# Kernel tuning notes

Measured on AMD Instinct MI355X. Metric: run time of the kernel, lower is better.

The kernel has to match this reference:

```python
import jax, jax.numpy as jnp
import numpy as np

B, L, D, P = 2, 1024, 256, 32

def setup_inputs() -> dict:
    key = jax.random.key(0)
    k1, k2, k3, k4, k5 = jax.random.split(key, 5)
    x = jax.random.normal(k1, (B, L, D), dtype=jnp.float32)
    s_in = 1.0 / np.sqrt(D)
    W_phase = jax.random.normal(k2, (D, P), dtype=jnp.float32) * s_in
    b_phase = jax.random.normal(k3, (P,), dtype=jnp.float32) * 0.01
    W_val = jax.random.normal(k4, (D, D), dtype=jnp.float32) * s_in
    b_val = jax.random.normal(k5, (D,), dtype=jnp.float32) * 0.01
    return {"x": x, "W_phase": W_phase, "b_phase": b_phase, "W_val": W_val, "b_val": b_val}

def reference(x, W_phase, b_phase, W_val, b_val):
    # phases: [B, L, P] in (-pi, pi)
    phases = jnp.tanh(x @ W_phase + b_phase) * jnp.float32(np.pi)
    # unit-magnitude complex phasors: [B, L, P]
    phasors = jnp.exp(1j * phases)  # complex64
    # values: [B, L, D]
    values = x @ W_val + b_val
    # bind value vector to each phasor via outer product: [B, L, P, D] complex64
    bound = phasors[..., None] * values[:, :, None, :].astype(jnp.complex64)
    # holographic memory = running sum over sequence position
    memory = jnp.cumsum(bound, axis=1)
    return (memory, phases, phasors)
```

## Files before the change

### kernel.cpp

```cpp
#include <hip/hip_runtime.h>
#include <math.h>

#define B_ 2
#define L_ 1024
#define D_ 256
#define P_ 32
#define NROW (B_*L_)
#define C_ 16
#define CL_ (L_/C_)
#define PIF 3.14159265358979323846f

typedef float nvf4 __attribute__((ext_vector_type(4)));
typedef float nvf2 __attribute__((ext_vector_type(2)));

__global__ __launch_bounds__(256) void k_proj3(
    const float* __restrict__ x, const float* __restrict__ Wp,
    const float* __restrict__ bp, const float* __restrict__ Wv,
    const float* __restrict__ bv, float* __restrict__ values,
    float* __restrict__ phases_out, float* __restrict__ phasor_out,
    float2* __restrict__ phasorT, int phasorMode, int hasPT)
{
    __shared__ float smem[5120];
    const int tid = threadIdx.x;

    if (blockIdx.x < NROW / 4) {
        const int row0 = blockIdx.x * 4;
        float*  xsv = smem;
        float4* red = (float4*)(smem + 1024);

        ((float4*)xsv)[tid] = ((const float4*)(x + (size_t)row0 * D_))[tid];
        __syncthreads();

        const int q  = tid >> 6;
        const int c4 = tid & 63;
        const float4* Wv4 = (const float4*)Wv;
        float4 acc[4];
        #pragma unroll
        for (int r = 0; r < 4; ++r) acc[r] = make_float4(0.f, 0.f, 0.f, 0.f);

        const int k0 = q * 64;
        #pragma unroll 4
        for (int kk = 0; kk < 64; ++kk) {
            const int k = k0 + kk;
            float4 w = Wv4[k * 64 + c4];
            #pragma unroll
            for (int r = 0; r < 4; ++r) {
                float xv = xsv[r * D_ + k];
                acc[r].x += xv * w.x; acc[r].y += xv * w.y;
                acc[r].z += xv * w.z; acc[r].w += xv * w.w;
            }
        }
        #pragma unroll
        for (int r = 0; r < 4; ++r) red[(r * 4 + q) * 64 + c4] = acc[r];
        __syncthreads();

        const int r2 = tid >> 6;
        float4 s0 = red[(r2 * 4 + 0) * 64 + c4];
        float4 s1 = red[(r2 * 4 + 1) * 64 + c4];
        float4 s2 = red[(r2 * 4 + 2) * 64 + c4];
        float4 s3 = red[(r2 * 4 + 3) * 64 + c4];
        const float4 b4 = ((const float4*)bv)[c4];
        float4 out;
        out.x = s0.x + s1.x + s2.x + s3.x + b4.x;
        out.y = s0.y + s1.y + s2.y + s3.y + b4.y;
        out.z = s0.z + s1.z + s2.z + s3.z + b4.z;
        out.w = s0.w + s1.w + s2.w + s3.w + b4.w;
        ((float4*)values)[(size_t)(row0 + r2) * 64 + c4] = out;
    } else {
        const int row0 = (blockIdx.x - NROW / 4) * 8;
        float* xs = smem;
        const float4* xg4 = (const float4*)(x + (size_t)row0 * D_);
        ((float4*)xs)[tid]       = xg4[tid];
        ((float4*)xs)[tid + 256] = xg4[tid + 256];
        __syncthreads();

        const int p  = tid & (P_ - 1);
        const int rr = tid >> 5;
        const float* xr = xs + rr * D_;
        float a = 0.f;
        #pragma unroll 8
        for (int k = 0; k < D_; ++k)
            a += xr[k] * Wp[k * P_ + p];
        float ph = tanhf(a + bp[p]) * PIF;
        const int row = row0 + rr;
        const int idx = row * P_ + p;
        phases_out[idx] = ph;
        float s, c;
        sincosf(ph, &s, &c);
        if (phasorMode == 0) {
            ((float2*)phasor_out)[idx] = make_float2(c, s);
        } else if (phasorMode == 1) {
            phasor_out[idx] = c;
        }
        if (hasPT) {
            const int b = row >> 10, l = row & (L_ - 1);
            phasorT[(b * P_ + p) * L_ + l] = make_float2(c, s);
        }
    }
}

__global__ __launch_bounds__(128) void k_partial(
    const float* __restrict__ values, const float* __restrict__ phases,
    const float2* __restrict__ phasorT, float4* __restrict__ S4, int hasPT)
{
    const int blk = blockIdx.x;
    const int c = blk & (C_ - 1);
    const int p = (blk >> 4) & (P_ - 1);
    const int b = blk >> 9;
    const int tid = threadIdx.x;
    const int l0 = c * CL_;

    __shared__ float2 pc[CL_];
    if (tid < CL_) {
        if (hasPT) {
            pc[tid] = phasorT[(b * P_ + p) * L_ + l0 + tid];
        } else {
            float ph = phases[(b * L_ + l0 + tid) * P_ + p];
            pc[tid] = make_float2(__cosf(ph), __sinf(ph));
        }
    }
    __syncthreads();

    const float2* v2 = (const float2*)(values + (size_t)(b * L_ + l0) * D_);
    float4 acc = make_float4(0.f, 0.f, 0.f, 0.f);
    #pragma unroll 8
    for (int i = 0; i < CL_; ++i) {
        float2 ph = pc[i];
        float2 v  = v2[i * (D_/2) + tid];
        acc.x += ph.x * v.x;
        acc.y += ph.y * v.x;
        acc.z += ph.x * v.y;
        acc.w += ph.y * v.y;
    }
    S4[((b * P_ + p) * C_ + c) * (D_/2) + tid] = acc;
}

__global__ __launch_bounds__(128) void k_scan(
    const float* __restrict__ values, const float* __restrict__ phases,
    const float2* __restrict__ phasorT, const float4* __restrict__ S4,
    float* __restrict__ mem, int mode, int hasPT)
{
    const int blk = blockIdx.x;
    const int c = blk & (C_ - 1);
    const int p = (blk >> 4) & (P_ - 1);
    const int b = blk >> 9;
    const int tid = threadIdx.x;
    const int l0 = c * CL_;

    __shared__ float2 pc[CL_];
    if (tid < CL_) {
        if (hasPT) {
            pc[tid] = phasorT[(b * P_ + p) * L_ + l0 + tid];
        } else {
            float ph = phases[(b * L_ + l0 + tid) * P_ + p];
            pc[tid] = make_float2(__cosf(ph), __sinf(ph));
        }
    }

    float4 carry = make_float4(0.f, 0.f, 0.f, 0.f);
    const float4* Sbase = S4 + (size_t)(b * P_ + p) * C_ * (D_/2) + tid;
    for (int cc = 0; cc < c; ++cc) {
        float4 s = Sbase[cc * (D_/2)];
        carry.x += s.x; carry.y += s.y; carry.z += s.z; carry.w += s.w;
    }
    __syncthreads();

    const float2* v2 = (const float2*)(values + (size_t)(b * L_ + l0) * D_);
    #pragma unroll 8
    for (int i = 0; i < CL_; ++i) {
        float2 ph = pc[i];
        float2 v  = v2[i * (D_/2) + tid];
        carry.x += ph.x * v.x;
        carry.y += ph.y * v.x;
        carry.z += ph.x * v.y;
        carry.w += ph.y * v.y;
        const size_t rowIdx = (size_t)(b * L_ + l0 + i) * P_ + p;
        if (mode == 0) {
            nvf4 cv = { carry.x, carry.y, carry.z, carry.w };
            __builtin_nontemporal_store(cv, (nvf4*)mem + rowIdx * (D_/2) + tid);
        } else {
            nvf2 cv = { carry.x, carry.z };
            __builtin_nontemporal_store(cv, (nvf2*)mem + rowIdx * (D_/2) + tid);
        }
    }
}

__global__ __launch_bounds__(128) void k_scan_rc(
    const float* __restrict__ values, const float* __restrict__ phases,
    float* __restrict__ mem, int mode)
{
    const int blk = blockIdx.x;
    const int c = blk & (C_ - 1);
    const int p = (blk >> 4) & (P_ - 1);
    const int b = blk >> 9;
    const int tid = threadIdx.x;
    const int l0 = c * CL_;

    const float2* vb = (const float2*)(values + (size_t)b * L_ * D_);
    float4 carry = make_float4(0.f, 0.f, 0.f, 0.f);
    for (int l = 0; l < l0; ++l) {
        float ph = phases[(b * L_ + l) * P_ + p];
        float s = __sinf(ph), cs = __cosf(ph);
        float2 v = vb[l * (D_/2) + tid];
        carry.x += cs * v.x; carry.y += s * v.x;
        carry.z += cs * v.y; carry.w += s * v.y;
    }
    for (int i = 0; i < CL_; ++i) {
        const int l = l0 + i;
        float ph = phases[(b * L_ + l) * P_ + p];
        float s = __sinf(ph), cs = __cosf(ph);
        float2 v = vb[l * (D_/2) + tid];
        carry.x += cs * v.x; carry.y += s * v.x;
        carry.z += cs * v.y; carry.w += s * v.y;
        const size_t rowIdx = (size_t)(b * L_ + l) * P_ + p;
        if (mode == 0) ((float4*)mem)[rowIdx * (D_/2) + tid] = carry;
        else ((float2*)mem)[rowIdx * (D_/2) + tid] = make_float2(carry.x, carry.z);
    }
}

extern "C" void kernel_launch(void* const* d_in, const int* in_sizes, int n_in,
                              void* d_out, int out_size, void* d_ws, size_t ws_size,
                              hipStream_t stream) {
    const float* x  = (const float*)d_in[0];
    const float* Wp = (const float*)d_in[1];
    const float* bp = (const float*)d_in[2];
    const float* Wv = (const float*)d_in[3];
    const float* bv = (const float*)d_in[4];
    float* out = (float*)d_out;

    const size_t nMemF = (size_t)2 * B_ * L_ * P_ * D_;
    const size_t nMemR = (size_t)B_ * L_ * P_ * D_;
    const size_t nPh   = (size_t)B_ * L_ * P_;

    int mode; size_t memFloats;
    if ((size_t)out_size >= nMemF + 3 * nPh) { mode = 0; memFloats = nMemF; }
    else                                     { mode = 1; memFloats = nMemR; }
    const bool memFits      = (size_t)out_size >= memFloats;
    const bool phasesInOut  = (size_t)out_size >= memFloats + nPh;
    const bool phasorsInOut =
        (size_t)out_size >= memFloats + nPh + (mode == 0 ? 2 * nPh : nPh);

    const size_t valB = (size_t)B_ * L_ * D_ * sizeof(float);
    const size_t phB  = nPh * sizeof(float);
    const size_t s4B  = (size_t)B_ * P_ * C_ * (D_/2) * sizeof(float4);
    const size_t ptB  = (size_t)B_ * P_ * L_ * sizeof(float2);
    float*  values   = (float*)d_ws;
    float*  phasesWs = (float*)((char*)d_ws + valB);
    float4* S4       = (float4*)((char*)d_ws + valB + phB);
    float2* phasorT  = (float2*)((char*)d_ws + valB + phB + s4B);

    float* phasesPtr = phasesInOut ? (out + memFloats)
                     : (ws_size >= valB + phB ? phasesWs : nullptr);
    if (phasesPtr == nullptr) return;

    float* phasorPtr = phasorsInOut ? (out + memFloats + nPh) : nullptr;
    const int phasorMode = phasorsInOut ? mode : 2;

    const bool pathA = ws_size >= valB + phB + s4B;
    const int  hasPT = (pathA && ws_size >= valB + phB + s4B + ptB) ? 1 : 0;

    k_proj3<<<NROW / 4 + NROW / 8, 256, 0, stream>>>(
        x, Wp, bp, Wv, bv, values, phasesPtr, phasorPtr, phasorT,
        phasorMode, hasPT);
    if (!memFits) return;

    if (pathA) {
        k_partial<<<B_ * P_ * C_, 128, 0, stream>>>(values, phasesPtr, phasorT,
                                                    S4, hasPT);
        k_scan<<<B_ * P_ * C_, 128, 0, stream>>>(values, phasesPtr, phasorT,
                                                 S4, out, mode, hasPT);
    } else {
        k_scan_rc<<<B_ * P_ * C_, 128, 0, stream>>>(values, phasesPtr, out, mode);
    }
}
```

Before: 110.6 us.

## Fuse partial-sum and scan kernels by recomputing chunk prefix per block

Replaces the two-pass chunked scan (partial sums into a workspace buffer, then a scan kernel that reads them) with one kernel. Each block recomputes its prefix carry directly from values over all earlier positions, using phasors staged in shared memory. This removes one launch and the S4 round trip through global memory. In exchange, later chunks redo up to the full sequence length of multiply-adds and value reads, so the work per block is uneven. It also adds a real-only (cosine) phasor path for mode 1.

Measured after the change: 151.3 us. 36.8% more time.

```diff
diff --git a/kernel.cpp b/kernel.cpp
--- a/kernel.cpp
+++ b/kernel.cpp
@@ -18,7 +18,7 @@
     const float* __restrict__ bp, const float* __restrict__ Wv,
     const float* __restrict__ bv, float* __restrict__ values,
     float* __restrict__ phases_out, float* __restrict__ phasor_out,
-    float2* __restrict__ phasorT, int phasorMode, int hasPT)
+    float* __restrict__ phasorT, int phasorMode, int mode, int hasPT)
 {
     __shared__ float smem[5120];
     const int tid = threadIdx.x;
@@ -94,14 +94,17 @@
         }
         if (hasPT) {
             const int b = row >> 10, l = row & (L_ - 1);
-            phasorT[(b * P_ + p) * L_ + l] = make_float2(c, s);
+            const size_t ti = (size_t)(b * P_ + p) * L_ + l;
+            if (mode == 1) phasorT[ti] = c;
+            else ((float2*)phasorT)[ti] = make_float2(c, s);
         }
     }
 }
 
-__global__ __launch_bounds__(128) void k_partial(
+__global__ __launch_bounds__(128) void k_scan_fused(
     const float* __restrict__ values, const float* __restrict__ phases,
-    const float2* __restrict__ phasorT, float4* __restrict__ S4, int hasPT)
+    const float* __restrict__ phasorT, float* __restrict__ mem,
+    int mode, int hasPT)
 {
     const int blk = blockIdx.x;
     const int c = blk & (C_ - 1);
@@ -109,112 +112,78 @@
     const int b = blk >> 9;
     const int tid = threadIdx.x;
     const int l0 = c * CL_;
-
-    __shared__ float2 pc[CL_];
-    if (tid < CL_) {
-        if (hasPT) {
-            pc[tid] = phasorT[(b * P_ + p) * L_ + l0 + tid];
+    const int bp = b * P_ + p;
+    const int nPre = l0 + CL_;
+
+    __shared__ float2 pc2[L_];
+    float* pc1 = (float*)pc2;
+
+    if (hasPT) {
+        if (mode == 1) {
+            const float4* src = (const float4*)(phasorT + (size_t)bp * L_);
+            for (int i = tid; i < nPre / 4; i += 128)
+                ((float4*)pc1)[i] = src[i];
         } else {
-            float ph = phases[(b * L_ + l0 + tid) * P_ + p];
-            pc[tid] = make_float2(__cosf(ph), __sinf(ph));
+            const float4* src =
+                (const float4*)((const float2*)phasorT + (size_t)bp * L_);
+            for (int i = tid; i < nPre / 2; i += 128)
+                ((float4*)pc2)[i] = src[i];
+        }
+    } else {
+        for (int l = tid; l < nPre; l += 128) {
+            float ph = phases[(b * L_ + l) * P_ + p];
+            if (mode == 1) pc1[l] = __cosf(ph);
+            else           pc2[l] = make_float2(__cosf(ph), __sinf(ph));
         }
     }
     __syncthreads();
 
-    const float2* v2 = (const float2*)(values + (size_t)(b * L_ + l0) * D_);
-    float4 acc = make_float4(0.f, 0.f, 0.f, 0.f);
-    #pragma unroll 8
-    for (int i = 0; i < CL_; ++i) {
-        float2 ph = pc[i];
-        float2 v  = v2[i * (D_/2) + tid];
-        acc.x += ph.x * v.x;
-        acc.y += ph.y * v.x;
-        acc.z += ph.x * v.y;
-        acc.w += ph.y * v.y;
-    }
-    S4[((b * P_ + p) * C_ + c) * (D_/2) + tid] = acc;
-}
-
-__global__ __launch_bounds__(128) void k_scan(
-    const float* __restrict__ values, const float* __restrict__ phases,
-    const float2* __restrict__ phasorT, const float4* __restrict__ S4,
-    float* __restrict__ mem, int mode, int hasPT)
-{
-    const int blk = blockIdx.x;
-    const int c = blk & (C_ - 1);
-    const int p = (blk >> 4) & (P_ - 1);
-    const int b = blk >> 9;
-    const int tid = threadIdx.x;
-    const int l0 = c * CL_;
-
-    __shared__ float2 pc[CL_];
-    if (tid < CL_) {
-        if (hasPT) {
-            pc[tid] = phasorT[(b * P_ + p) * L_ + l0 + tid];
-        } else {
-            float ph = phases[(b * L_ + l0 + tid) * P_ + p];
-            pc[tid] = make_float2(__cosf(ph), __sinf(ph));
-        }
-    }
-
-    float4 carry = make_float4(0.f, 0.f, 0.f, 0.f);
-    const float4* Sbase = S4 + (size_t)(b * P_ + p) * C_ * (D_/2) + tid;
-    for (int cc = 0; cc < c; ++cc) {
-        float4 s = Sbase[cc * (D_/2)];
-        carry.x += s.x; carry.y += s.y; carry.z += s.z; carry.w += s.w;
-    }
-    __syncthreads();
-
-    const float2* v2 = (const float2*)(values + (size_t)(b * L_ + l0) * D_);
-    #pragma unroll 8
-    for (int i = 0; i < CL_; ++i) {
-        float2 ph = pc[i];
-        float2 v  = v2[i * (D_/2) + tid];
-        carry.x += ph.x * v.x;
-        carry.y += ph.y * v.x;
-        carry.z += ph.x * v.y;
-        carry.w += ph.y * v.y;
-        const size_t rowIdx = (size_t)(b * L_ + l0 + i) * P_ + p;
-        if (mode == 0) {
+    const float2* v2 = (const float2*)(values + (size_t)b * L_ * D_);
+
+    if (mode == 1) {
+        float cx = 0.f, cz = 0.f;
+        #pragma unroll 8
+        for (int l = 0; l < l0; ++l) {
+            float pcv = pc1[l];
+            float2 v  = v2[(size_t)l * (D_/2) + tid];
+            cx += pcv * v.x;
+            cz += pcv * v.y;
+        }
+        #pragma unroll 8
+        for (int i = 0; i < CL_; ++i) {
+            const int l = l0 + i;
+            float pcv = pc1[l];
+            float2 v  = v2[(size_t)l * (D_/2) + tid];
+            cx += pcv * v.x;
+            cz += pcv * v.y;
+            nvf2 cv = { cx, cz };
+            __builtin_nontemporal_store(
+                cv, (nvf2*)mem + ((size_t)(b * L_ + l) * P_ + p) * (D_/2) + tid);
+        }
+    } else {
+        float4 carry = make_float4(0.f, 0.f, 0.f, 0.f);
+        #pragma unroll 8
+        for (int l = 0; l < l0; ++l) {
+            float2 ph = pc2[l];
+            float2 v  = v2[(size_t)l * (D_/2) + tid];
+            carry.x += ph.x * v.x;
+            carry.y += ph.y * v.x;
+            carry.z += ph.x * v.y;
+            carry.w += ph.y * v.y;
+        }
+        #pragma unroll 8
+        for (int i = 0; i < CL_; ++i) {
+            const int l = l0 + i;
+            float2 ph = pc2[l];
+            float2 v  = v2[(size_t)l * (D_/2) + tid];
+            carry.x += ph.x * v.x;
+            carry.y += ph.y * v.x;
+            carry.z += ph.x * v.y;
+            carry.w += ph.y * v.y;
             nvf4 cv = { carry.x, carry.y, carry.z, carry.w };
-            __builtin_nontemporal_store(cv, (nvf4*)mem + rowIdx * (D_/2) + tid);
-        } else {
-            nvf2 cv = { carry.x, carry.z };
-            __builtin_nontemporal_store(cv, (nvf2*)mem + rowIdx * (D_/2) + tid);
-        }
-    }
-}
-
-__global__ __launch_bounds__(128) void k_scan_rc(
-    const float* __restrict__ values, const float* __restrict__ phases,
-    float* __restrict__ mem, int mode)
-{
-    const int blk = blockIdx.x;
-    const int c = blk & (C_ - 1);
-    const int p = (blk >> 4) & (P_ - 1);
-    const int b = blk >> 9;
-    const int tid = threadIdx.x;
-    const int l0 = c * CL_;
-
-    const float2* vb = (const float2*)(values + (size_t)b * L_ * D_);
-    float4 carry = make_float4(0.f, 0.f, 0.f, 0.f);
-    for (int l = 0; l < l0; ++l) {
-        float ph = phases[(b * L_ + l) * P_ + p];
-        float s = __sinf(ph), cs = __cosf(ph);
-        float2 v = vb[l * (D_/2) + tid];
-        carry.x += cs * v.x; carry.y += s * v.x;
-        carry.z += cs * v.y; carry.w += s * v.y;
-    }
-    for (int i = 0; i < CL_; ++i) {
-        const int l = l0 + i;
-        float ph = phases[(b * L_ + l) * P_ + p];
-        float s = __sinf(ph), cs = __cosf(ph);
-        float2 v = vb[l * (D_/2) + tid];
-        carry.x += cs * v.x; carry.y += s * v.x;
-        carry.z += cs * v.y; carry.w += s * v.y;
-        const size_t rowIdx = (size_t)(b * L_ + l) * P_ + p;
-        if (mode == 0) ((float4*)mem)[rowIdx * (D_/2) + tid] = carry;
-        else ((float2*)mem)[rowIdx * (D_/2) + tid] = make_float2(carry.x, carry.z);
+            __builtin_nontemporal_store(
+                cv, (nvf4*)mem + ((size_t)(b * L_ + l) * P_ + p) * (D_/2) + tid);
+        }
     }
 }
 
@@ -242,12 +211,10 @@
 
     const size_t valB = (size_t)B_ * L_ * D_ * sizeof(float);
     const size_t phB  = nPh * sizeof(float);
-    const size_t s4B  = (size_t)B_ * P_ * C_ * (D_/2) * sizeof(float4);
-    const size_t ptB  = (size_t)B_ * P_ * L_ * sizeof(float2);
-    float*  values   = (float*)d_ws;
-    float*  phasesWs = (float*)((char*)d_ws + valB);
-    float4* S4       = (float4*)((char*)d_ws + valB + phB);
-    float2* phasorT  = (float2*)((char*)d_ws + valB + phB + s4B);
+    const size_t ptB  = nPh * (mode == 0 ? sizeof(float2) : sizeof(float));
+    float* values   = (float*)d_ws;
+    float* phasesWs = (float*)((char*)d_ws + valB);
+    float* phasorT  = (float*)((char*)d_ws + valB + phB);
 
     float* phasesPtr = phasesInOut ? (out + memFloats)
                      : (ws_size >= valB + phB ? phasesWs : nullptr);
@@ -256,20 +223,13 @@
     float* phasorPtr = phasorsInOut ? (out + memFloats + nPh) : nullptr;
     const int phasorMode = phasorsInOut ? mode : 2;
 
-    const bool pathA = ws_size >= valB + phB + s4B;
-    const int  hasPT = (pathA && ws_size >= valB + phB + s4B + ptB) ? 1 : 0;
+    const int hasPT = (ws_size >= valB + phB + ptB) ? 1 : 0;
 
     k_proj3<<<NROW / 4 + NROW / 8, 256, 0, stream>>>(
         x, Wp, bp, Wv, bv, values, phasesPtr, phasorPtr, phasorT,
-        phasorMode, hasPT);
+        phasorMode, mode, hasPT);
     if (!memFits) return;
 
-    if (pathA) {
-        k_partial<<<B_ * P_ * C_, 128, 0, stream>>>(values, phasesPtr, phasorT,
-                                                    S4, hasPT);
-        k_scan<<<B_ * P_ * C_, 128, 0, stream>>>(values, phasesPtr, phasorT,
-                                                 S4, out, mode, hasPT);
-    } else {
-        k_scan_rc<<<B_ * P_ * C_, 128, 0, stream>>>(values, phasesPtr, out, mode);
-    }
+    k_scan_fused<<<B_ * P_ * C_, 128, 0, stream>>>(values, phasesPtr, phasorT,
+                                                   out, mode, hasPT);
 }
```
